# Optimization experiments

Hardware: AMD Instinct MI355X
Metric: run time of the kernel (lower is better)

The kernel has to match this reference:

```python
import jax, jax.numpy as jnp
import numpy as np

EPS = 1e-12  # torch F.normalize default eps


def setup_inputs() -> dict:
    key = jax.random.key(0)
    k1, k2, k3 = jax.random.split(key, 3)
    ns, d_in, n_feat, n_classes = 16384, 512, 256, 1000
    x = jax.random.normal(k1, (ns, d_in), dtype=jnp.float32)
    W = jax.random.normal(k2, (d_in, n_feat), dtype=jnp.float32) * 0.05
    # class prototypes: L2-normalized embeddings, one per seen class (seen_c == n_classes)
    means = jax.random.normal(k3, (n_classes, n_feat), dtype=jnp.float32)
    means = means / jnp.maximum(jnp.linalg.norm(means, axis=1, keepdims=True), EPS)
    return {"x": x, "W": W, "means": means, "t": 0}


def reference(x, W, means, t):
    # forward_training: backbone + L2 normalization along feature dim
    feats = x @ W                                   # [ns, n_feat]
    preds = feats / jnp.maximum(jnp.linalg.norm(feats, axis=1, keepdims=True), EPS)
    # deployment forward: nearest prototype by negative dot product
    # original: per-sample dist = -means @ pred^T; dist.min(0) -> class index
    dist = -(preds @ means.T)                       # [ns, seen_c]
    classpred = jnp.argmin(dist, axis=1)            # first min on ties, matches torch
    n_classes = means.shape[0]
    out = jax.nn.one_hot(classpred, n_classes, dtype=jnp.float32)  # [ns, n_classes]
    return out
```

## Files before the change

### kernel.cpp

```cpp
#include <hip/hip_runtime.h>
#include <float.h>

#define NS   16384
#define K1   512
#define F    256
#define NC   1000
#define SPB  32
#define NTHR 512
#define NBLK (NS / SPB)


typedef _Float16 half8 __attribute__((ext_vector_type(8)));
typedef float    float4v __attribute__((ext_vector_type(4)));

#define WH_OFF 0
#define WL_OFF 131072
#define MH_OFF 262144
#define ML_OFF (262144 + 262144)

__global__ void prep_w(const float* __restrict__ W, _Float16* __restrict__ ws) {
    int g    = blockIdx.x * blockDim.x + threadIdx.x;
    int lane = g & 63, tile = g >> 6;
    int ks = tile >> 4, nt = tile & 15;
    int k0 = ks * 32 + (lane >> 4) * 8;
    int n  = nt * 16 + (lane & 15);
    _Float16 h[8], l[8];
#pragma unroll
    for (int j = 0; j < 8; ++j) {
        float v = W[(size_t)(k0 + j) * F + n] * 16.0f;
        _Float16 hi = (_Float16)v;
        h[j] = hi;
        l[j] = (_Float16)(v - (float)hi);
    }
    _Float16* dh = ws + WH_OFF + (size_t)g * 8;
    _Float16* dl = ws + WL_OFF + (size_t)g * 8;
#pragma unroll
    for (int j = 0; j < 8; ++j) { dh[j] = h[j]; dl[j] = l[j]; }
}

__global__ void prep_m(const float* __restrict__ means, _Float16* __restrict__ ws) {
    int g    = blockIdx.x * blockDim.x + threadIdx.x;
    int lane = g & 63, tile = g >> 6;
    int ks = tile >> 6, gt = tile & 63;
    int k0 = ks * 32 + (lane >> 4) * 8;
    int c  = gt * 16 + (lane & 15);
    _Float16 h[8], l[8];
#pragma unroll
    for (int j = 0; j < 8; ++j) {
        float v = (c < NC) ? means[(size_t)c * F + k0 + j] * 16.0f : 0.0f;
        _Float16 hi = (_Float16)v;
        h[j] = hi;
        l[j] = (_Float16)(v - (float)hi);
    }
    _Float16* dh = ws + MH_OFF + (size_t)g * 8;
    _Float16* dl = ws + ML_OFF + (size_t)g * 8;
#pragma unroll
    for (int j = 0; j < 8; ++j) { dh[j] = h[j]; dl[j] = l[j]; }
}

#define MFMA(a, b, c) __builtin_amdgcn_mfma_f32_16x16x32_f16((a), (b), (c), 0, 0, 0)

__attribute__((amdgpu_flat_work_group_size(NTHR, NTHR), amdgpu_waves_per_eu(2, 4)))
__global__ void fused_mfma(const float* __restrict__ x,
                           const _Float16* __restrict__ ws,
                           float* __restrict__ out) {
    __shared__ _Float16 xsh[2][32][44];
    __shared__ _Float16 xsl[2][32][44];
    __shared__ _Float16 fh[32][264];
    __shared__ _Float16 fl[32][264];
    __shared__ float cand_v[32][8];
    __shared__ int   cand_i[32][8];
    __shared__ int   bidx[32];

    const int tid  = threadIdx.x;
    const int lane = tid & 63;
    const int w    = tid >> 6;
    const int quad = lane >> 4;
    const int cl   = lane & 15;
    const int s0   = blockIdx.x * SPB;

    const int xrow = tid >> 4;
    const int xc   = (tid & 15) * 2;

    float4v acc1[2][2];
#pragma unroll
    for (int p = 0; p < 2; ++p)
#pragma unroll
        for (int mt = 0; mt < 2; ++mt)
            acc1[p][mt] = (float4v){0.f, 0.f, 0.f, 0.f};

    float2 xv = *reinterpret_cast<const float2*>(x + (size_t)(s0 + xrow) * K1 + xc);

    for (int ks = 0; ks < 16; ++ks) {
        const int buf = ks & 1;
        {
            float vx = xv.x * 8.0f, vy = xv.y * 8.0f;
            _Float16 hx = (_Float16)vx, hy = (_Float16)vy;
            xsh[buf][xrow][xc]     = hx;
            xsh[buf][xrow][xc + 1] = hy;
            xsl[buf][xrow][xc]     = (_Float16)(vx - (float)hx);
            xsl[buf][xrow][xc + 1] = (_Float16)(vy - (float)hy);
        }
        __syncthreads();
        if (ks < 15)
            xv = *reinterpret_cast<const float2*>(
                x + (size_t)(s0 + xrow) * K1 + (ks + 1) * 32 + xc);

        half8 ah[2], al[2];
#pragma unroll
        for (int mt = 0; mt < 2; ++mt) {
            ah[mt] = *reinterpret_cast<const half8*>(&xsh[buf][mt * 16 + cl][quad * 8]);
            al[mt] = *reinterpret_cast<const half8*>(&xsl[buf][mt * 16 + cl][quad * 8]);
        }
#pragma unroll
        for (int p = 0; p < 2; ++p) {
            const int tile = ks * 16 + (w * 2 + p);
            half8 bh = *reinterpret_cast<const half8*>(
                ws + WH_OFF + ((size_t)tile * 64 + lane) * 8);
            half8 bl = *reinterpret_cast<const half8*>(
                ws + WL_OFF + ((size_t)tile * 64 + lane) * 8);
#pragma unroll
            for (int mt = 0; mt < 2; ++mt) {
                acc1[p][mt] = MFMA(ah[mt], bh, acc1[p][mt]);
                acc1[p][mt] = MFMA(ah[mt], bl, acc1[p][mt]);
                acc1[p][mt] = MFMA(al[mt], bh, acc1[p][mt]);
            }
        }
    }

#pragma unroll
    for (int p = 0; p < 2; ++p)
#pragma unroll
        for (int mt = 0; mt < 2; ++mt)
#pragma unroll
            for (int r = 0; r < 4; ++r) {
                int srow = mt * 16 + quad * 4 + r;
                int n    = (w * 2 + p) * 16 + cl;
                float v  = acc1[p][mt][r];
                _Float16 hi = (_Float16)v;
                fh[srow][n] = hi;
                fl[srow][n] = (_Float16)(v - (float)hi);
            }
    __syncthreads();

    float4v acc2[2][8];
#pragma unroll
    for (int mt = 0; mt < 2; ++mt)
#pragma unroll
        for (int nt = 0; nt < 8; ++nt)
            acc2[mt][nt] = (float4v){0.f, 0.f, 0.f, 0.f};

    for (int ks = 0; ks < 8; ++ks) {
        half8 fah[2], fal[2];
#pragma unroll
        for (int mt = 0; mt < 2; ++mt) {
            fah[mt] = *reinterpret_cast<const half8*>(
                &fh[mt * 16 + cl][ks * 32 + quad * 8]);
            fal[mt] = *reinterpret_cast<const half8*>(
                &fl[mt * 16 + cl][ks * 32 + quad * 8]);
        }
#pragma unroll
        for (int nt = 0; nt < 8; ++nt) {
            const int tile = ks * 64 + (w * 8 + nt);
            half8 mh = *reinterpret_cast<const half8*>(
                ws + MH_OFF + ((size_t)tile * 64 + lane) * 8);
            half8 ml = *reinterpret_cast<const half8*>(
                ws + ML_OFF + ((size_t)tile * 64 + lane) * 8);
#pragma unroll
            for (int mt = 0; mt < 2; ++mt) {
                acc2[mt][nt] = MFMA(fah[mt], mh, acc2[mt][nt]);
                acc2[mt][nt] = MFMA(fah[mt], ml, acc2[mt][nt]);
                acc2[mt][nt] = MFMA(fal[mt], mh, acc2[mt][nt]);
            }
        }
    }

#pragma unroll
    for (int mt = 0; mt < 2; ++mt)
#pragma unroll
        for (int r = 0; r < 4; ++r) {
            float v  = -FLT_MAX;
            int   ix = 0x7FFFFFFF;
#pragma unroll
            for (int nt = 0; nt < 8; ++nt) {
                int c = (w * 8 + nt) * 16 + cl;
                if (c < NC) {
                    float sc = acc2[mt][nt][r];
                    if (sc > v) { v = sc; ix = c; }
                }
            }
#pragma unroll
            for (int off = 1; off < 16; off <<= 1) {
                float ov = __shfl_xor(v, off, 64);
                int   oi = __shfl_xor(ix, off, 64);
                if (ov > v || (ov == v && oi < ix)) { v = ov; ix = oi; }
            }
            if (cl == 0) {
                int srow = mt * 16 + quad * 4 + r;
                cand_v[srow][w] = v;
                cand_i[srow][w] = ix;
            }
        }
    __syncthreads();

    if (tid < 32) {
        float v  = cand_v[tid][0];
        int   ix = cand_i[tid][0];
#pragma unroll
        for (int q = 1; q < 8; ++q) {
            float ov = cand_v[tid][q];
            int   oi = cand_i[tid][q];
            if (ov > v || (ov == v && oi < ix)) { v = ov; ix = oi; }
        }
        bidx[tid] = ix;
    }
    __syncthreads();

    const int NF4 = NC / 4;
    for (int q = tid; q < SPB * NF4; q += NTHR) {
        int row   = q / NF4;
        int c4    = q - row * NF4;
        int b     = bidx[row];
        int cbase = c4 * 4;
        float4 v;
        v.x = (cbase + 0 == b) ? 1.f : 0.f;
        v.y = (cbase + 1 == b) ? 1.f : 0.f;
        v.z = (cbase + 2 == b) ? 1.f : 0.f;
        v.w = (cbase + 3 == b) ? 1.f : 0.f;
        *reinterpret_cast<float4*>(out + (size_t)(s0 + row) * NC + cbase) = v;
    }
}

extern "C" void kernel_launch(void* const* d_in, const int* in_sizes, int n_in,
                              void* d_out, int out_size, void* d_ws, size_t ws_size,
                              hipStream_t stream) {
    const float* x     = (const float*)d_in[0];
    const float* W     = (const float*)d_in[1];
    const float* means = (const float*)d_in[2];
    float* out         = (float*)d_out;
    _Float16* ws       = (_Float16*)d_ws;

    prep_w<<<64, 256, 0, stream>>>(W, ws);
    prep_m<<<128, 256, 0, stream>>>(means, ws);
    fused_mfma<<<NBLK, NTHR, 0, stream>>>(x, ws, out);
}
```

Measured before the change: 137.6 us.

## Merge prep kernels, widen x staging, prefetch means fragments, share LDS

Folds the two weight and prototype split-precision prep kernels into one launch to remove one launch overhead. The first GEMM now stages 64 K-columns of x per barrier using float4 loads and half4 LDS stores, halving the number of syncs. The second GEMM software-prefetches the next means fragment and the next feature fragment from LDS, so loads overlap the MFMAs. LDS is unioned into one buffer, with the candidate arrays aliased over the x buffers, and waves_per_eu is relaxed. Together these raise register pressure and add aliasing hazards.

After: 169.1 us. 22.9% more time.

```diff
diff --git a/kernel.cpp b/kernel.cpp
--- a/kernel.cpp
+++ b/kernel.cpp
@@ -11,6 +11,7 @@
 
 
 typedef _Float16 half8 __attribute__((ext_vector_type(8)));
+typedef _Float16 half4 __attribute__((ext_vector_type(4)));
 typedef float    float4v __attribute__((ext_vector_type(4)));
 
 #define WH_OFF 0
@@ -18,59 +19,56 @@
 #define MH_OFF 262144
 #define ML_OFF (262144 + 262144)
 
-__global__ void prep_w(const float* __restrict__ W, _Float16* __restrict__ ws) {
-    int g    = blockIdx.x * blockDim.x + threadIdx.x;
-    int lane = g & 63, tile = g >> 6;
-    int ks = tile >> 4, nt = tile & 15;
-    int k0 = ks * 32 + (lane >> 4) * 8;
-    int n  = nt * 16 + (lane & 15);
-    _Float16 h[8], l[8];
-#pragma unroll
-    for (int j = 0; j < 8; ++j) {
-        float v = W[(size_t)(k0 + j) * F + n] * 16.0f;
-        _Float16 hi = (_Float16)v;
-        h[j] = hi;
-        l[j] = (_Float16)(v - (float)hi);
-    }
-    _Float16* dh = ws + WH_OFF + (size_t)g * 8;
-    _Float16* dl = ws + WL_OFF + (size_t)g * 8;
-#pragma unroll
-    for (int j = 0; j < 8; ++j) { dh[j] = h[j]; dl[j] = l[j]; }
+__global__ void prep_frags(const float* __restrict__ W,
+                           const float* __restrict__ means,
+                           _Float16* __restrict__ ws) {
+    int g = blockIdx.x * blockDim.x + threadIdx.x;
+    if (g < 16384) {
+        int lane = g & 63, tile = g >> 6;
+        int ks = tile >> 4, nt = tile & 15;
+        int k0 = ks * 32 + (lane >> 4) * 8;
+        int n  = nt * 16 + (lane & 15);
+        _Float16* dh = ws + WH_OFF + (size_t)g * 8;
+        _Float16* dl = ws + WL_OFF + (size_t)g * 8;
+#pragma unroll
+        for (int j = 0; j < 8; ++j) {
+            float v = W[(size_t)(k0 + j) * F + n] * 16.0f;
+            _Float16 hi = (_Float16)v;
+            dh[j] = hi;
+            dl[j] = (_Float16)(v - (float)hi);
+        }
+    } else {
+        int gm = g - 16384;
+        int lane = gm & 63, tile = gm >> 6;
+        int ks = tile >> 6, gt = tile & 63;
+        int k0 = ks * 32 + (lane >> 4) * 8;
+        int c  = gt * 16 + (lane & 15);
+        _Float16* dh = ws + MH_OFF + (size_t)gm * 8;
+        _Float16* dl = ws + ML_OFF + (size_t)gm * 8;
+#pragma unroll
+        for (int j = 0; j < 8; ++j) {
+            float v = (c < NC) ? means[(size_t)c * F + k0 + j] * 16.0f : 0.0f;
+            _Float16 hi = (_Float16)v;
+            dh[j] = hi;
+            dl[j] = (_Float16)(v - (float)hi);
+        }
+    }
 }
 
-__global__ void prep_m(const float* __restrict__ means, _Float16* __restrict__ ws) {
-    int g    = blockIdx.x * blockDim.x + threadIdx.x;
-    int lane = g & 63, tile = g >> 6;
-    int ks = tile >> 6, gt = tile & 63;
-    int k0 = ks * 32 + (lane >> 4) * 8;
-    int c  = gt * 16 + (lane & 15);
-    _Float16 h[8], l[8];
-#pragma unroll
-    for (int j = 0; j < 8; ++j) {
-        float v = (c < NC) ? means[(size_t)c * F + k0 + j] * 16.0f : 0.0f;
-        _Float16 hi = (_Float16)v;
-        h[j] = hi;
-        l[j] = (_Float16)(v - (float)hi);
-    }
-    _Float16* dh = ws + MH_OFF + (size_t)g * 8;
-    _Float16* dl = ws + ML_OFF + (size_t)g * 8;
-#pragma unroll
-    for (int j = 0; j < 8; ++j) { dh[j] = h[j]; dl[j] = l[j]; }
-}
-
 #define MFMA(a, b, c) __builtin_amdgcn_mfma_f32_16x16x32_f16((a), (b), (c), 0, 0, 0)
 
-__attribute__((amdgpu_flat_work_group_size(NTHR, NTHR), amdgpu_waves_per_eu(2, 4)))
+__attribute__((amdgpu_flat_work_group_size(NTHR, NTHR), amdgpu_waves_per_eu(2, 8)))
 __global__ void fused_mfma(const float* __restrict__ x,
                            const _Float16* __restrict__ ws,
                            float* __restrict__ out) {
-    __shared__ _Float16 xsh[2][32][44];
-    __shared__ _Float16 xsl[2][32][44];
-    __shared__ _Float16 fh[32][264];
-    __shared__ _Float16 fl[32][264];
-    __shared__ float cand_v[32][8];
-    __shared__ int   cand_i[32][8];
-    __shared__ int   bidx[32];
+    __shared__ __align__(16) unsigned char smem[52224];
+    _Float16 (*xsh)[32][72] = reinterpret_cast<_Float16 (*)[32][72]>(smem);
+    _Float16 (*xsl)[32][72] = reinterpret_cast<_Float16 (*)[32][72]>(smem + 9216);
+    _Float16 (*fh)[264]     = reinterpret_cast<_Float16 (*)[264]>(smem + 18432);
+    _Float16 (*fl)[264]     = reinterpret_cast<_Float16 (*)[264]>(smem + 35328);
+    float (*cand_v)[8]      = reinterpret_cast<float (*)[8]>(smem);
+    int   (*cand_i)[8]      = reinterpret_cast<int (*)[8]>(smem + 1024);
+    int*  bidx              = reinterpret_cast<int*>(smem + 2048);
 
     const int tid  = threadIdx.x;
     const int lane = tid & 63;
@@ -80,7 +78,7 @@
     const int s0   = blockIdx.x * SPB;
 
     const int xrow = tid >> 4;
-    const int xc   = (tid & 15) * 2;
+    const int xc4  = (tid & 15) * 4;
 
     float4v acc1[2][2];
 #pragma unroll
@@ -89,41 +87,47 @@
         for (int mt = 0; mt < 2; ++mt)
             acc1[p][mt] = (float4v){0.f, 0.f, 0.f, 0.f};
 
-    float2 xv = *reinterpret_cast<const float2*>(x + (size_t)(s0 + xrow) * K1 + xc);
-
-    for (int ks = 0; ks < 16; ++ks) {
-        const int buf = ks & 1;
+    float4 xv = *reinterpret_cast<const float4*>(x + (size_t)(s0 + xrow) * K1 + xc4);
+
+    for (int ks8 = 0; ks8 < 8; ++ks8) {
+        const int buf = ks8 & 1;
         {
-            float vx = xv.x * 8.0f, vy = xv.y * 8.0f;
-            _Float16 hx = (_Float16)vx, hy = (_Float16)vy;
-            xsh[buf][xrow][xc]     = hx;
-            xsh[buf][xrow][xc + 1] = hy;
-            xsl[buf][xrow][xc]     = (_Float16)(vx - (float)hx);
-            xsl[buf][xrow][xc + 1] = (_Float16)(vy - (float)hy);
+            float v0 = xv.x * 8.0f, v1 = xv.y * 8.0f, v2 = xv.z * 8.0f, v3 = xv.w * 8.0f;
+            _Float16 h0 = (_Float16)v0, h1 = (_Float16)v1, h2 = (_Float16)v2, h3 = (_Float16)v3;
+            *reinterpret_cast<half4*>(&xsh[buf][xrow][xc4]) = (half4){h0, h1, h2, h3};
+            *reinterpret_cast<half4*>(&xsl[buf][xrow][xc4]) =
+                (half4){(_Float16)(v0 - (float)h0), (_Float16)(v1 - (float)h1),
+                        (_Float16)(v2 - (float)h2), (_Float16)(v3 - (float)h3)};
         }
         __syncthreads();
-        if (ks < 15)
-            xv = *reinterpret_cast<const float2*>(
-                x + (size_t)(s0 + xrow) * K1 + (ks + 1) * 32 + xc);
-
-        half8 ah[2], al[2];
-#pragma unroll
-        for (int mt = 0; mt < 2; ++mt) {
-            ah[mt] = *reinterpret_cast<const half8*>(&xsh[buf][mt * 16 + cl][quad * 8]);
-            al[mt] = *reinterpret_cast<const half8*>(&xsl[buf][mt * 16 + cl][quad * 8]);
-        }
-#pragma unroll
-        for (int p = 0; p < 2; ++p) {
-            const int tile = ks * 16 + (w * 2 + p);
-            half8 bh = *reinterpret_cast<const half8*>(
-                ws + WH_OFF + ((size_t)tile * 64 + lane) * 8);
-            half8 bl = *reinterpret_cast<const half8*>(
-                ws + WL_OFF + ((size_t)tile * 64 + lane) * 8);
+        if (ks8 < 7)
+            xv = *reinterpret_cast<const float4*>(
+                x + (size_t)(s0 + xrow) * K1 + (ks8 + 1) * 64 + xc4);
+
+#pragma unroll
+        for (int s2 = 0; s2 < 2; ++s2) {
+            const int ks = ks8 * 2 + s2;
+            half8 ah[2], al[2];
 #pragma unroll
             for (int mt = 0; mt < 2; ++mt) {
-                acc1[p][mt] = MFMA(ah[mt], bh, acc1[p][mt]);
-                acc1[p][mt] = MFMA(ah[mt], bl, acc1[p][mt]);
-                acc1[p][mt] = MFMA(al[mt], bh, acc1[p][mt]);
+                ah[mt] = *reinterpret_cast<const half8*>(
+                    &xsh[buf][mt * 16 + cl][s2 * 32 + quad * 8]);
+                al[mt] = *reinterpret_cast<const half8*>(
+                    &xsl[buf][mt * 16 + cl][s2 * 32 + quad * 8]);
+            }
+#pragma unroll
+            for (int p = 0; p < 2; ++p) {
+                const int tile = ks * 16 + (w * 2 + p);
+                half8 bh = *reinterpret_cast<const half8*>(
+                    ws + WH_OFF + ((size_t)tile * 64 + lane) * 8);
+                half8 bl = *reinterpret_cast<const half8*>(
+                    ws + WL_OFF + ((size_t)tile * 64 + lane) * 8);
+#pragma unroll
+                for (int mt = 0; mt < 2; ++mt) {
+                    acc1[p][mt] = MFMA(ah[mt], bh, acc1[p][mt]);
+                    acc1[p][mt] = MFMA(ah[mt], bl, acc1[p][mt]);
+                    acc1[p][mt] = MFMA(al[mt], bh, acc1[p][mt]);
+                }
             }
         }
     }
@@ -150,29 +154,45 @@
         for (int nt = 0; nt < 8; ++nt)
             acc2[mt][nt] = (float4v){0.f, 0.f, 0.f, 0.f};
 
+    const _Float16* mhb = ws + MH_OFF + (size_t)(w * 8) * 64 * 8 + (size_t)lane * 8;
+    const _Float16* mlb = ws + ML_OFF + (size_t)(w * 8) * 64 * 8 + (size_t)lane * 8;
+
+    half8 fahC[2], falC[2], fahN[2], falN[2];
+#pragma unroll
+    for (int mt = 0; mt < 2; ++mt) {
+        fahC[mt] = *reinterpret_cast<const half8*>(&fh[mt * 16 + cl][quad * 8]);
+        falC[mt] = *reinterpret_cast<const half8*>(&fl[mt * 16 + cl][quad * 8]);
+    }
+    half8 cmh = *reinterpret_cast<const half8*>(mhb);
+    half8 cml = *reinterpret_cast<const half8*>(mlb);
+
     for (int ks = 0; ks < 8; ++ks) {
-        half8 fah[2], fal[2];
-#pragma unroll
-        for (int mt = 0; mt < 2; ++mt) {
-            fah[mt] = *reinterpret_cast<const half8*>(
-                &fh[mt * 16 + cl][ks * 32 + quad * 8]);
-            fal[mt] = *reinterpret_cast<const half8*>(
-                &fl[mt * 16 + cl][ks * 32 + quad * 8]);
+        if (ks < 7) {
+#pragma unroll
+            for (int mt = 0; mt < 2; ++mt) {
+                fahN[mt] = *reinterpret_cast<const half8*>(
+                    &fh[mt * 16 + cl][(ks + 1) * 32 + quad * 8]);
+                falN[mt] = *reinterpret_cast<const half8*>(
+                    &fl[mt * 16 + cl][(ks + 1) * 32 + quad * 8]);
+            }
         }
 #pragma unroll
         for (int nt = 0; nt < 8; ++nt) {
-            const int tile = ks * 64 + (w * 8 + nt);
-            half8 mh = *reinterpret_cast<const half8*>(
-                ws + MH_OFF + ((size_t)tile * 64 + lane) * 8);
-            half8 ml = *reinterpret_cast<const half8*>(
-                ws + ML_OFF + ((size_t)tile * 64 + lane) * 8);
+            const int t  = ks * 8 + nt;
+            const int tn = (t + 1 < 64) ? t + 1 : 63;
+            const size_t noff = (size_t)(((tn >> 3) * 64 + (tn & 7)) * 64) * 8;
+            half8 nmh = *reinterpret_cast<const half8*>(mhb + noff);
+            half8 nml = *reinterpret_cast<const half8*>(mlb + noff);
 #pragma unroll
             for (int mt = 0; mt < 2; ++mt) {
-                acc2[mt][nt] = MFMA(fah[mt], mh, acc2[mt][nt]);
-                acc2[mt][nt] = MFMA(fah[mt], ml, acc2[mt][nt]);
-                acc2[mt][nt] = MFMA(fal[mt], mh, acc2[mt][nt]);
-            }
-        }
+                acc2[mt][nt] = MFMA(fahC[mt], cmh, acc2[mt][nt]);
+                acc2[mt][nt] = MFMA(fahC[mt], cml, acc2[mt][nt]);
+                acc2[mt][nt] = MFMA(falC[mt], cmh, acc2[mt][nt]);
+            }
+            cmh = nmh; cml = nml;
+        }
+#pragma unroll
+        for (int mt = 0; mt < 2; ++mt) { fahC[mt] = fahN[mt]; falC[mt] = falN[mt]; }
     }
 
 #pragma unroll
@@ -240,7 +260,6 @@
     float* out         = (float*)d_out;
     _Float16* ws       = (_Float16*)d_ws;
 
-    prep_w<<<64, 256, 0, stream>>>(W, ws);
-    prep_m<<<128, 256, 0, stream>>>(means, ws);
+    prep_frags<<<192, 256, 0, stream>>>(W, means, ws);
     fused_mfma<<<NBLK, NTHR, 0, stream>>>(x, ws, out);
 }
```
